# Kernel optimization log

Hardware: AMD Instinct MI355X
Metric: run time of the kernel (lower is better)

Reference implementation:

```python
import jax, jax.numpy as jnp
import numpy as np

EMBED_DIM = 768
NUM_HEADS = 12
PROJ_DIM = EMBED_DIM // NUM_HEADS  # 64
M_FEATURES = 128
EPS = 1e-6


def _orthogonal_projection(key, m, d):
    # Faithful to create_projection_matrix(scaling=0): stacked transposed Q-factors
    # of iid gaussian blocks, rescaled by chi-distributed row norms.
    nb_full_blocks = m // d
    keys = jax.random.split(key, nb_full_blocks + 2)
    blocks = []
    for i in range(nb_full_blocks):
        q, _ = jnp.linalg.qr(jax.random.normal(keys[i], (d, d)))
        blocks.append(q.T)
    rem = m - nb_full_blocks * d
    if rem > 0:
        q, _ = jnp.linalg.qr(jax.random.normal(keys[nb_full_blocks], (d, d)))
        blocks.append(q.T[:rem])
    final = jnp.vstack(blocks)
    multiplier = jnp.linalg.norm(jax.random.normal(keys[-1], (m, d)), axis=1)
    return multiplier[:, None] * final


def setup_inputs() -> dict:
    key = jax.random.key(0)
    ks = jax.random.split(key, 8)
    B, L, E = 4, 4096, EMBED_DIM
    s = 1.0 / np.sqrt(E)
    inp = {
        "x": jax.random.normal(ks[0], (B, L, E), jnp.float32),
        "Wq": jax.random.normal(ks[1], (E, E), jnp.float32) * s,
        "bq": jnp.zeros((E,), jnp.float32),
        "Wk": jax.random.normal(ks[2], (E, E), jnp.float32) * s,
        "bk": jnp.zeros((E,), jnp.float32),
        "Wv": jax.random.normal(ks[3], (E, E), jnp.float32) * s,
        "bv": jnp.zeros((E,), jnp.float32),
        "Wo": jax.random.normal(ks[4], (E, E), jnp.float32) * s,
        "bo": jnp.zeros((E,), jnp.float32),
        "proj": _orthogonal_projection(ks[5], M_FEATURES, PROJ_DIM),
    }
    return inp


def _softmax_kernel(data, projection_matrix):
    # data: [B, L, H, D]; projection_matrix: [M, D]
    data_normalizer = 1.0 / jnp.sqrt(jnp.sqrt(jnp.float32(PROJ_DIM)))
    data = data_normalizer * data
    ratio = 1.0 / jnp.sqrt(jnp.float32(projection_matrix.shape[0]))
    data_dash = jnp.einsum("blhd,md->blhm", data, projection_matrix)
    diag_data = jnp.sum(jnp.square(data), axis=-1, keepdims=True) / 2.0  # [B,L,H,1]
    stab = jnp.max(data_dash, axis=-1, keepdims=True)
    return ratio * (jnp.exp(data_dash - diag_data - stab) + EPS)


def reference(x, Wq, bq, Wk, bk, Wv, bv, Wo, bo, proj):
    B, L, E = x.shape
    H, D = NUM_HEADS, PROJ_DIM

    def split_heads(t):
        return t.reshape(B, L, H, D)

    q = split_heads(x @ Wq + bq)
    k = split_heads(x @ Wk + bk)
    v = split_heads(x @ Wv + bv)

    q_prime = _softmax_kernel(q, proj)  # [B,L,H,M]
    k_prime = _softmax_kernel(k, proj)  # [B,L,H,M]

    # Linear-attention numerator/denominator (O(L) in sequence length).
    kvs = jnp.einsum("blhm,blhd->bhmd", k_prime, v)          # [B,H,M,D]
    num = jnp.einsum("blhm,bhmd->blhd", q_prime, kvs)        # [B,L,H,D]
    ks_sum = jnp.sum(k_prime, axis=1)                         # [B,H,M]
    den = jnp.einsum("blhm,bhm->blh", q_prime, ks_sum)        # [B,L,H]
    attention = num / den[..., None]                          # [B,L,H,D]

    # Faithful to source: transpose to [B,H,L,D] then reshape to [B,-1,E].
    concat = jnp.transpose(attention, (0, 2, 1, 3)).reshape(B, -1, E)
    return concat @ Wo + bo
```

## Files before the change

### kernel.cpp

```cpp
#include <hip/hip_runtime.h>

typedef _Float16 f16;
typedef __attribute__((ext_vector_type(8))) _Float16 half8;
typedef __attribute__((ext_vector_type(4))) _Float16 half4;
typedef __attribute__((ext_vector_type(4))) float f32x4;

#define DEVINL static __device__ __forceinline__

constexpr float NORMALIZER = 0.35355339059327373f;
constexpr float RATIO      = 0.08838834764831845f;
constexpr float FEPS       = 1e-6f;

constexpr size_t OFF_WQKVT = 0;
constexpr size_t OFF_WOT   = OFF_WQKVT + (size_t)2304*768*2;
constexpr size_t OFF_PROJF = OFF_WOT   + (size_t)768*768*2;
constexpr size_t OFF_KS    = OFF_PROJF + (size_t)128*64*2;
constexpr size_t OFF_KSP   = OFF_KS    + (size_t)48*128*4;
constexpr size_t OFF_DEN   = OFF_KSP   + (size_t)48*64*128*4;
constexpr size_t OFF_KVST  = OFF_DEN   + (size_t)48*4096*4;
constexpr size_t OFF_KVSP  = OFF_KVST  + (size_t)48*64*128*2;
constexpr size_t OFF_X16   = OFF_KVSP  + (size_t)8*48*128*64*4;
constexpr size_t OFF_ATT   = OFF_X16;
constexpr size_t OFF_Q16   = OFF_X16 + (size_t)16384*768*2;
constexpr size_t OFF_K16   = OFF_Q16 + (size_t)16384*768*2;
constexpr size_t OFF_VT    = OFF_K16 + (size_t)16384*768*2;
constexpr size_t OFF_KPT   = OFF_VT  + (size_t)16384*768*2;

DEVINL void gload_lds16(const f16* g, f16* lds) {
  __builtin_amdgcn_global_load_lds(
      (const __attribute__((address_space(1))) void*)g,
      (__attribute__((address_space(3))) void*)lds, 16, 0, 0);
}

#define VMCNT(n)  asm volatile("s_waitcnt vmcnt(" #n ")" ::: "memory")
#define LGKMCNT0  asm volatile("s_waitcnt lgkmcnt(0)" ::: "memory")
#define SCHEDB    __builtin_amdgcn_sched_barrier(0)
#define BAR       __builtin_amdgcn_s_barrier()

DEVINL void gemm192_core(const f16* __restrict__ Ag, const f16* __restrict__ Bg,
                         f16* smem, f32x4 (&acc)[8][3], int w, int lane)
{
  constexpr int NT = 12;
  const int wm = w >> 2, wn = w & 3;
  const int c = lane & 15, g16 = lane >> 4;
  const int tid = threadIdx.x;

#pragma unroll
  for (int i = 0; i < 8; ++i)
#pragma unroll
    for (int j = 0; j < 3; ++j)
      acc[i][j] = f32x4{0.f, 0.f, 0.f, 0.f};

  auto SA = [&](int tt, int kh, f16* buf) {
    f16* dst = buf + kh * 8192;
#pragma unroll
    for (int u = 0; u < 2; ++u) {
      const int id = u * 512 + tid;
      const int r = id >> 2, sg = id & 3;
      const int seg = sg ^ ((r >> 1) & 3);
      gload_lds16(Ag + (size_t)r * 768 + tt * 64 + kh * 32 + seg * 8,
                  dst + (u * 512 + w * 64) * 8);
    }
  };
  auto SB = [&](int tt, f16* buf) {
    f16* dst = buf + 16384;
#pragma unroll
    for (int u = 0; u < 3; ++u) {
      const int id = u * 512 + tid;
      const int r = id >> 3, sg = id & 7;
      const int seg = sg ^ (r & 7);
      gload_lds16(Bg + (size_t)r * 768 + tt * 64 + seg * 8,
                  dst + (u * 512 + w * 64) * 8);
    }
  };
  auto RDA = [&](const f16* buf, int kh, int mh, half8 (&av)[4]) {
    const f16* base = buf + kh * 8192;
#pragma unroll
    for (int i = 0; i < 4; ++i) {
      const int r = wm * 128 + mh * 64 + i * 16 + c;
      av[i] = *(const half8*)(base + r * 32 + ((g16 ^ ((r >> 1) & 3)) << 3));
    }
  };
  auto RDB = [&](const f16* buf, int kh, half8 (&bv)[3]) {
#pragma unroll
    for (int j = 0; j < 3; ++j) {
      const int r = wn * 48 + j * 16 + c;
      const int s = kh * 4 + g16;
      bv[j] = *(const half8*)(buf + 16384 + r * 64 + ((s ^ (r & 7)) << 3));
    }
  };

  SA(0, 0, smem); SB(0, smem); SA(0, 1, smem);
  VMCNT(0);
  BAR; SCHEDB;

#pragma unroll 1
  for (int t = 0; t < NT; ++t) {
    f16* bufR = smem + (t & 1) * 28672;
    f16* bufW = smem + ((t & 1) ^ 1) * 28672;
    const bool st = (t + 1) < NT;
    half8 av[4], bv[3];

    RDA(bufR, 0, 0, av); RDB(bufR, 0, bv);
    if (st) SA(t + 1, 0, bufW);
    SCHEDB; BAR; LGKMCNT0; SCHEDB;
    __builtin_amdgcn_s_setprio(1);
#pragma unroll
    for (int i = 0; i < 4; ++i)
#pragma unroll
      for (int j = 0; j < 3; ++j)
        acc[i][j] = __builtin_amdgcn_mfma_f32_16x16x32_f16(av[i], bv[j], acc[i][j], 0, 0, 0);
    __builtin_amdgcn_s_setprio(0);
    BAR; SCHEDB;
    RDA(bufR, 0, 1, av);
    if (st) SB(t + 1, bufW);
    SCHEDB; BAR; LGKMCNT0; SCHEDB;
    __builtin_amdgcn_s_setprio(1);
#pragma unroll
    for (int i = 0; i < 4; ++i)
#pragma unroll
      for (int j = 0; j < 3; ++j)
        acc[4 + i][j] = __builtin_amdgcn_mfma_f32_16x16x32_f16(av[i], bv[j], acc[4 + i][j], 0, 0, 0);
    __builtin_amdgcn_s_setprio(0);
    if (st) { VMCNT(5); } else { VMCNT(0); }
    BAR; SCHEDB;
    RDA(bufR, 1, 0, av); RDB(bufR, 1, bv);
    if (st) SA(t + 1, 1, bufW);
    SCHEDB; BAR; LGKMCNT0; SCHEDB;
    __builtin_amdgcn_s_setprio(1);
#pragma unroll
    for (int i = 0; i < 4; ++i)
#pragma unroll
      for (int j = 0; j < 3; ++j)
        acc[i][j] = __builtin_amdgcn_mfma_f32_16x16x32_f16(av[i], bv[j], acc[i][j], 0, 0, 0);
    __builtin_amdgcn_s_setprio(0);
    BAR; SCHEDB;
    RDA(bufR, 1, 1, av);
    SCHEDB; BAR; LGKMCNT0; SCHEDB;
    __builtin_amdgcn_s_setprio(1);
#pragma unroll
    for (int i = 0; i < 4; ++i)
#pragma unroll
      for (int j = 0; j < 3; ++j)
        acc[4 + i][j] = __builtin_amdgcn_mfma_f32_16x16x32_f16(av[i], bv[j], acc[4 + i][j], 0, 0, 0);
    __builtin_amdgcn_s_setprio(0);
    if (st) { VMCNT(2); }
    BAR; SCHEDB;
  }
}

__global__ __launch_bounds__(512, 2) void k_gemm_qkv5(const f16* __restrict__ X16, const f16* __restrict__ WT,
    const float* __restrict__ bq, const float* __restrict__ bk, const float* __restrict__ bv,
    f16* __restrict__ Qo, f16* __restrict__ Ko, f16* __restrict__ VT)
{
  __shared__ f16 smem[57344];
  f32x4 acc[8][3];
  const int lin = blockIdx.x;
  const int xcd = lin & 7, chunk = lin >> 3;
  const int bx = xcd * 8 + chunk / 12;
  const int by = chunk % 12;
  const int brow0 = bx * 256;
  const int t = threadIdx.x, w = t >> 6, lane = t & 63;
  gemm192_core(X16 + (size_t)brow0 * 768, WT + (size_t)by * 192 * 768, smem, acc, w, lane);

  const int wm = w >> 2, wn = w & 3;
  const int c = lane & 15, g16 = lane >> 4;
  const int which = by >> 2;
  const int colhdr = (by & 3) * 192;
  const float* bias = which == 0 ? bq : (which == 1 ? bk : bv);
  float bb[3];
#pragma unroll
  for (int j = 0; j < 3; ++j) bb[j] = bias[colhdr + wn * 48 + j * 16 + c];

  f16* ep = smem;
  if (which < 2) {
    f16* QK = which == 0 ? Qo : Ko;
#pragma unroll 1
    for (int p = 0; p < 2; ++p) {
      __syncthreads();
      if (wm == p) {
#pragma unroll
        for (int ii = 0; ii < 8; ++ii)
#pragma unroll
          for (int j = 0; j < 3; ++j)
#pragma unroll
            for (int r = 0; r < 4; ++r)
              ep[((ii >> 2) * 64 + (ii & 3) * 16 + g16 * 4 + r) * 200 + wn * 48 + j * 16 + c]
                  = (f16)(acc[ii][j][r] + bb[j]);
      }
      __syncthreads();
      const int row = t >> 2, sg = (t & 3) * 48;
      f16* dst = QK + (size_t)(brow0 + p * 128 + row) * 768 + colhdr + sg;
      const f16* sp = ep + row * 200 + sg;
#pragma unroll
      for (int u = 0; u < 6; ++u) *(half8*)(dst + u * 8) = *(const half8*)(sp + u * 8);
    }
  } else {
    const int bIdx = brow0 >> 12;
#pragma unroll 1
    for (int p = 0; p < 2; ++p) {
      __syncthreads();
      if (wm == p) {
#pragma unroll
        for (int ii = 0; ii < 8; ++ii)
#pragma unroll
          for (int j = 0; j < 3; ++j)
#pragma unroll
            for (int r = 0; r < 4; ++r)
              ep[(wn * 48 + j * 16 + c) * 136 + (ii >> 2) * 64 + (ii & 3) * 16 + g16 * 4 + r]
                  = (f16)(acc[ii][j][r] + bb[j]);
      }
      __syncthreads();
      if (t < 384) {
        const int cl = t >> 1, sg = (t & 1) * 64;
        const int vcol = colhdr + cl;
        const int h = vcol >> 6, d = vcol & 63;
        f16* dst = VT + ((size_t)(bIdx * 12 + h) * 64 + d) * 4096 + (brow0 & 4095) + p * 128 + sg;
        const f16* sp = ep + cl * 136 + sg;
#pragma unroll
        for (int u = 0; u < 8; ++u) *(half8*)(dst + u * 8) = *(const half8*)(sp + u * 8);
      }
    }
  }
}

__global__ __launch_bounds__(512, 2) void k_gemm_out5(const f16* __restrict__ ATT, const f16* __restrict__ WOT,
    const float* __restrict__ bo, float* __restrict__ out)
{
  __shared__ f16 smem[57344];
  f32x4 acc[8][3];
  const int lin = blockIdx.x;
  const int xcd = lin & 7, chunk = lin >> 3;
  const int bx = xcd * 8 + (chunk >> 2);
  const int by = chunk & 3;
  const int brow0 = bx * 256;
  const int t = threadIdx.x, w = t >> 6, lane = t & 63;
  gemm192_core(ATT + (size_t)brow0 * 768, WOT + (size_t)by * 192 * 768, smem, acc, w, lane);

  const int wm = w >> 2, wn = w & 3;
  const int c = lane & 15, g16 = lane >> 4;
  float bb[3];
#pragma unroll
  for (int j = 0; j < 3; ++j) bb[j] = bo[by * 192 + wn * 48 + j * 16 + c];
#pragma unroll
  for (int ii = 0; ii < 8; ++ii) {
    const int row0 = brow0 + wm * 128 + (ii >> 2) * 64 + (ii & 3) * 16 + g16 * 4;
#pragma unroll
    for (int j = 0; j < 3; ++j) {
      const int col = by * 192 + wn * 48 + j * 16 + c;
#pragma unroll
      for (int r = 0; r < 4; ++r)
        out[(size_t)(row0 + r) * 768 + col] = acc[ii][j][r] + bb[j];
    }
  }
}

template<int BN>
DEVINL void gemm_tile(const f16* A, int lda, const f16* Bt, int ldb, int K,
                      f16* As, f16* Bs, f32x4 (&acc)[4][BN/32])
{
  constexpr int NF = BN/32;
  const int t = threadIdx.x;
  const int w = t >> 6, lane = t & 63;
  const int g = lane >> 4, c = lane & 15;
  const int wr = w >> 1, wc = w & 1;
  const int srow = lane >> 2;
  const int sseg = (lane & 3) * 8;

#pragma unroll
  for (int i = 0; i < 4; ++i)
#pragma unroll
    for (int j = 0; j < NF; ++j)
      acc[i][j] = f32x4{0.f, 0.f, 0.f, 0.f};

  for (int k0 = 0; k0 < K; k0 += 32) {
#pragma unroll
    for (int r = 0; r < 2; ++r) {
      const int rowblk = (w + 4*r) * 16;
      gload_lds16(A + (size_t)(rowblk + srow) * lda + k0 + sseg, As + rowblk*32);
    }
#pragma unroll
    for (int r = 0; r < BN/64; ++r) {
      const int rowblk = (w + 4*r) * 16;
      gload_lds16(Bt + (size_t)(rowblk + srow) * ldb + k0 + sseg, Bs + rowblk*32);
    }
    __syncthreads();
    half8 av[4], bv[NF];
#pragma unroll
    for (int i = 0; i < 4; ++i)
      av[i] = *(const half8*)(As + (wr*64 + i*16 + c)*32 + g*8);
#pragma unroll
    for (int j = 0; j < NF; ++j)
      bv[j] = *(const half8*)(Bs + (wc*(BN/2) + j*16 + c)*32 + g*8);
#pragma unroll
    for (int i = 0; i < 4; ++i)
#pragma unroll
      for (int j = 0; j < NF; ++j)
        acc[i][j] = __builtin_amdgcn_mfma_f32_16x16x32_f16(av[i], bv[j], acc[i][j], 0, 0, 0);
    __syncthreads();
  }
}

__global__ __launch_bounds__(256) void k_cast_x(const float* __restrict__ X, f16* __restrict__ X16)
{
  const size_t i = ((size_t)blockIdx.x*256 + threadIdx.x) * 4;
  const float4 v = *(const float4*)(X + i);
  half4 h;
  h[0] = (f16)v.x; h[1] = (f16)v.y; h[2] = (f16)v.z; h[3] = (f16)v.w;
  *(half4*)(X16 + i) = h;
}

__global__ __launch_bounds__(256) void k_transpose_w(const float* __restrict__ W, f16* __restrict__ Wt)
{
  __shared__ float ls[64][65];
  const int t = threadIdx.x;
  const int k0 = blockIdx.x*64, n0 = blockIdx.y*64;
#pragma unroll
  for (int it = 0; it < 4; ++it) {
    const int r = it*16 + (t >> 4);
    const int cs = (t & 15) * 4;
    const float4 v = *(const float4*)(W + (size_t)(k0 + r)*768 + n0 + cs);
    ls[r][cs+0] = v.x; ls[r][cs+1] = v.y; ls[r][cs+2] = v.z; ls[r][cs+3] = v.w;
  }
  __syncthreads();
  const int n = t >> 2;
  const int seg = (t & 3) * 16;
  half8 ov[2];
#pragma unroll
  for (int i = 0; i < 16; ++i) ov[i>>3][i&7] = (f16)ls[seg + i][n];
  f16* dst = Wt + (size_t)(n0 + n)*768 + k0 + seg;
  *(half8*)dst = ov[0];
  *(half8*)(dst + 8) = ov[1];
}

__global__ __launch_bounds__(256) void k_cast_proj(const float* __restrict__ P, f16* __restrict__ PF)
{
  const int i = blockIdx.x*256 + threadIdx.x;
  PF[i] = (f16)(NORMALIZER * P[i]);
}

DEVINL void feat_common(const f16* base, const f16* PROJF,
                        f16* qs, f16* ps, float* dd, float* diag_s)
{
  const int t = threadIdx.x, w = t >> 6, lane = t & 63;
#pragma unroll
  for (int it = 0; it < 2; ++it) {
    const int rowblk = it*32 + w*8;
    gload_lds16(base + (size_t)(rowblk + (lane>>3))*768 + (lane&7)*8, qs + rowblk*64);
  }
#pragma unroll
  for (int it = 0; it < 4; ++it) {
    const int rowblk = it*32 + w*8;
    gload_lds16(PROJF + (size_t)(rowblk + (lane>>3))*64 + (lane&7)*8, ps + rowblk*64);
  }
  __syncthreads();
  if (t < 64) {
    float s = 0.f;
    for (int d = 0; d < 64; ++d) { const float qv = (float)qs[t*64 + d]; s += qv*qv; }
    diag_s[t] = 0.0625f * s;
  }
  const int g = lane >> 4, c = lane & 15;
  const int wr = w >> 1, wc = w & 1;
  f32x4 facc[2][4];
#pragma unroll
  for (int i = 0; i < 2; ++i)
#pragma unroll
    for (int j = 0; j < 4; ++j) facc[i][j] = f32x4{0.f,0.f,0.f,0.f};
#pragma unroll
  for (int kk = 0; kk < 2; ++kk) {
    half8 av[2], bv[4];
#pragma unroll
    for (int i = 0; i < 2; ++i) av[i] = *(const half8*)(qs + (wr*32 + i*16 + c)*64 + kk*32 + g*8);
#pragma unroll
    for (int j = 0; j < 4; ++j) bv[j] = *(const half8*)(ps + (wc*64 + j*16 + c)*64 + kk*32 + g*8);
#pragma unroll
    for (int i = 0; i < 2; ++i)
#pragma unroll
      for (int j = 0; j < 4; ++j)
        facc[i][j] = __builtin_amdgcn_mfma_f32_16x16x32_f16(av[i], bv[j], facc[i][j], 0, 0, 0);
  }
#pragma unroll
  for (int i = 0; i < 2; ++i)
#pragma unroll
    for (int j = 0; j < 4; ++j)
#pragma unroll
      for (int r = 0; r < 4; ++r)
        dd[(wr*32 + i*16 + g*4 + r)*129 + wc*64 + j*16 + c] = facc[i][j][r];
  __syncthreads();
}

__global__ __launch_bounds__(256) void k_kfeat(const f16* __restrict__ Kin, const f16* __restrict__ PROJF,
    f16* __restrict__ KPT, float* __restrict__ KSP)
{
  __shared__ f16 qs[64*64];
  __shared__ f16 ps[128*64];
  __shared__ float dd[64*129];
  __shared__ float diag_s[64];
  const int t = threadIdx.x;
  const int lb = blockIdx.x, bh = blockIdx.y;
  const int b = bh / 12, h = bh - b*12;
  feat_common(Kin + ((size_t)(b*4096 + lb*64))*768 + h*64, PROJF, qs, ps, dd, diag_s);
  const int l = t >> 2, s = t & 3;
  float v[32];
#pragma unroll
  for (int j = 0; j < 32; ++j) v[j] = dd[l*129 + s*32 + j];
  float mx = v[0];
#pragma unroll
  for (int j = 1; j < 32; ++j) mx = fmaxf(mx, v[j]);
  mx = fmaxf(mx, __shfl_xor(mx, 1));
  mx = fmaxf(mx, __shfl_xor(mx, 2));
  const float off = diag_s[l] + mx;
#pragma unroll
  for (int j = 0; j < 32; ++j) dd[l*129 + s*32 + j] = RATIO * (__expf(v[j] - off) + FEPS);
  __syncthreads();
  if (t < 128) {
    float sm = 0.f;
    for (int l2 = 0; l2 < 64; ++l2) sm += dd[l2*129 + t];
    KSP[((size_t)bh*64 + lb)*128 + t] = sm;
  }
  const int m = t >> 1, hf = t & 1;
  half8 ov[4];
#pragma unroll
  for (int i2 = 0; i2 < 32; ++i2) ov[i2>>3][i2&7] = (f16)dd[(hf*32 + i2)*129 + m];
  f16* dst = KPT + ((size_t)bh*128 + m)*4096 + lb*64 + hf*32;
#pragma unroll
  for (int q8 = 0; q8 < 4; ++q8) *(half8*)(dst + q8*8) = ov[q8];
}

__global__ __launch_bounds__(256) void k_kvs(const f16* __restrict__ KPT, const f16* __restrict__ VT,
    float* __restrict__ KVSP)
{
  __shared__ f16 As[128*32], Bs[64*32];
  f32x4 acc[4][2];
  const int chunk = blockIdx.x, bh = blockIdx.y;
  gemm_tile<64>(KPT + (size_t)bh*128*4096 + chunk*512, 4096,
                VT  + (size_t)bh*64*4096  + chunk*512, 4096, 512, As, Bs, acc);
  const int t = threadIdx.x, w = t>>6, lane = t&63, g = lane>>4, c = lane&15;
  const int wr = w>>1, wc = w&1;
  float* dst = KVSP + (size_t)(chunk*48 + bh)*128*64;
#pragma unroll
  for (int i = 0; i < 4; ++i) {
    const int row0 = wr*64 + i*16 + g*4;
#pragma unroll
    for (int j = 0; j < 2; ++j) {
      const int col = wc*32 + j*16 + c;
#pragma unroll
      for (int r = 0; r < 4; ++r) dst[(size_t)(row0 + r)*64 + col] = acc[i][j][r];
    }
  }
}

__global__ __launch_bounds__(256) void k_reduce(const float* __restrict__ KVSP, const float* __restrict__ KSP,
    f16* __restrict__ KVST, float* __restrict__ KS)
{
  const int i = blockIdx.x*256 + threadIdx.x;
  if (i < 48*128*64) {
    const int bh = i >> 13, md = i & 8191, m = md >> 6, d = md & 63;
    float s = 0.f;
#pragma unroll
    for (int c = 0; c < 8; ++c) s += KVSP[((size_t)(c*48 + bh)*128 + m)*64 + d];
    KVST[((size_t)bh*64 + d)*128 + m] = (f16)s;
  }
  if (i < 48*128) {
    const int bh = i >> 7, m = i & 127;
    float s = 0.f;
#pragma unroll 8
    for (int lb = 0; lb < 64; ++lb) s += KSP[((size_t)bh*64 + lb)*128 + m];
    KS[i] = s;
  }
}

__global__ __launch_bounds__(256) void k_qfn(const f16* __restrict__ Q, const f16* __restrict__ PROJF,
    const float* __restrict__ KS, const f16* __restrict__ KVST, f16* __restrict__ ATT)
{
  __shared__ f16 qs[64*64];
  __shared__ f16 ps[128*64];
  __shared__ float dd[64*129];
  __shared__ float diag_s[64];
  __shared__ float den_s[64];
  __shared__ f16 qp[64*128];
  __shared__ float ks_s[128];
  const int t = threadIdx.x;
  const int lb = blockIdx.x, bh = blockIdx.y;
  const int b = bh / 12, h = bh - b*12;
  if (t < 128) ks_s[t] = KS[bh*128 + t];
  feat_common(Q + ((size_t)(b*4096 + lb*64))*768 + h*64, PROJF, qs, ps, dd, diag_s);

  const int w = t >> 6, lane = t & 63, g16 = lane >> 4, c = lane & 15;
  const int wr = w >> 1, wc = w & 1;
  half8 bv2[2][4];
#pragma unroll
  for (int j = 0; j < 2; ++j) {
    const int d = wc*32 + j*16 + c;
#pragma unroll
    for (int kk = 0; kk < 4; ++kk)
      bv2[j][kk] = *(const half8*)(KVST + (size_t)bh*8192 + d*128 + kk*32 + g16*8);
  }

  const int l = t >> 2, s = t & 3;
  float v[32];
#pragma unroll
  for (int j = 0; j < 32; ++j) v[j] = dd[l*129 + s*32 + j];
  float mx = v[0];
#pragma unroll
  for (int j = 1; j < 32; ++j) mx = fmaxf(mx, v[j]);
  mx = fmaxf(mx, __shfl_xor(mx, 1));
  mx = fmaxf(mx, __shfl_xor(mx, 2));
  const float off = diag_s[l] + mx;
  half8 ov[4];
  float dp = 0.f;
#pragma unroll
  for (int j = 0; j < 32; ++j) {
    const float e = RATIO * (__expf(v[j] - off) + FEPS);
    ov[j>>3][j&7] = (f16)e;
    dp += e * ks_s[s*32 + j];
  }
  dp += __shfl_xor(dp, 1);
  dp += __shfl_xor(dp, 2);
  if (s == 0) den_s[l] = dp;
#pragma unroll
  for (int k = 0; k < 4; ++k)
    *(half8*)(qp + l*128 + (((4*s + k) ^ (l & 7)) << 3)) = ov[k];
  __syncthreads();

  f32x4 acc2[2][2];
#pragma unroll
  for (int i = 0; i < 2; ++i)
#pragma unroll
    for (int j = 0; j < 2; ++j) acc2[i][j] = f32x4{0.f,0.f,0.f,0.f};
#pragma unroll
  for (int kk = 0; kk < 4; ++kk) {
    half8 av2[2];
#pragma unroll
    for (int i = 0; i < 2; ++i) {
      const int l2 = wr*32 + i*16 + c;
      av2[i] = *(const half8*)(qp + l2*128 + (((kk*4 + g16) ^ (l2 & 7)) << 3));
    }
#pragma unroll
    for (int i = 0; i < 2; ++i)
#pragma unroll
      for (int j = 0; j < 2; ++j)
        acc2[i][j] = __builtin_amdgcn_mfma_f32_16x16x32_f16(av2[i], bv2[j][kk], acc2[i][j], 0, 0, 0);
  }

  f16* ep = ps;
#pragma unroll
  for (int i = 0; i < 2; ++i)
#pragma unroll
    for (int j = 0; j < 2; ++j)
#pragma unroll
      for (int r = 0; r < 4; ++r) {
        const int l3 = wr*32 + i*16 + g16*4 + r;
        ep[l3*72 + wc*32 + j*16 + c] = (f16)(acc2[i][j][r] / den_s[l3]);
      }
  __syncthreads();
  const int row = t >> 2, sg = (t & 3) * 16;
  f16* dst = ATT + ((size_t)bh*4096 + lb*64 + row)*64 + sg;
  const f16* sp = ep + row*72 + sg;
  *(half8*)dst = *(const half8*)sp;
  *(half8*)(dst + 8) = *(const half8*)(sp + 8);
}

extern "C" void kernel_launch(void* const* d_in, const int* in_sizes, int n_in,
                              void* d_out, int out_size, void* d_ws, size_t ws_size,
                              hipStream_t stream)
{
  const float* x    = (const float*)d_in[0];
  const float* Wq   = (const float*)d_in[1];
  const float* bq   = (const float*)d_in[2];
  const float* Wk   = (const float*)d_in[3];
  const float* bk   = (const float*)d_in[4];
  const float* Wv   = (const float*)d_in[5];
  const float* bv   = (const float*)d_in[6];
  const float* Wo   = (const float*)d_in[7];
  const float* bo   = (const float*)d_in[8];
  const float* proj = (const float*)d_in[9];
  float* out = (float*)d_out;
  char* ws = (char*)d_ws;

  f16*   WQKVT = (f16*)(ws + OFF_WQKVT);
  f16*   WOT   = (f16*)(ws + OFF_WOT);
  f16*   PROJF = (f16*)(ws + OFF_PROJF);
  float* KS    = (float*)(ws + OFF_KS);
  float* KSP   = (float*)(ws + OFF_KSP);
  f16*   KVST  = (f16*)(ws + OFF_KVST);
  float* KVSP  = (float*)(ws + OFF_KVSP);
  f16*   X16   = (f16*)(ws + OFF_X16);
  f16*   ATT   = (f16*)(ws + OFF_ATT);
  f16*   Q16   = (f16*)(ws + OFF_Q16);
  f16*   K16   = (f16*)(ws + OFF_K16);
  f16*   VT    = (f16*)(ws + OFF_VT);
  f16*   KPT   = (f16*)(ws + OFF_KPT);

  k_cast_x<<<12288, 256, 0, stream>>>(x, X16);
  k_transpose_w<<<dim3(12,12), 256, 0, stream>>>(Wq, WQKVT);
  k_transpose_w<<<dim3(12,12), 256, 0, stream>>>(Wk, WQKVT + (size_t)768*768);
  k_transpose_w<<<dim3(12,12), 256, 0, stream>>>(Wv, WQKVT + (size_t)2*768*768);
  k_transpose_w<<<dim3(12,12), 256, 0, stream>>>(Wo, WOT);
  k_cast_proj<<<32, 256, 0, stream>>>(proj, PROJF);

  k_gemm_qkv5<<<768, 512, 0, stream>>>(X16, WQKVT, bq, bk, bv, Q16, K16, VT);
  k_kfeat<<<dim3(64,48), 256, 0, stream>>>(K16, PROJF, KPT, KSP);
  k_kvs<<<dim3(8,48), 256, 0, stream>>>(KPT, VT, KVSP);
  k_reduce<<<1536, 256, 0, stream>>>(KVSP, KSP, KVST, KS);
  k_qfn<<<dim3(64,48), 256, 0, stream>>>(Q16, PROJF, KS, KVST, ATT);
  k_gemm_out5<<<256, 512, 0, stream>>>(ATT, WOT, bo, out);
}
```

Measured before the change: 251.5 us.

## Shrink GEMM tiles to 128 rows, raise occupancy, split KVS chunks, fuse weight transposes

The QKV and output GEMMs move from 256x192 tiles with 64-wide K steps to 128x192 tiles with 32-wide K steps. This cuts LDS and accumulator use so four blocks fit per CU, and launches twice as many blocks for better load balance on the GPU. The pipeline is simplified to one barrier and one vmcnt(0) per K step, dropping the finer-grained scheduling barriers. KVS is also split into 16 sequence chunks instead of 8, and the four weight transposes are merged into one launch. In exchange, the smaller tiles reuse less data per block and the simpler pipeline overlaps loads with compute less.

```diff
diff --git a/kernel.cpp b/kernel.cpp
--- a/kernel.cpp
+++ b/kernel.cpp
@@ -16,10 +16,9 @@
 constexpr size_t OFF_PROJF = OFF_WOT   + (size_t)768*768*2;
 constexpr size_t OFF_KS    = OFF_PROJF + (size_t)128*64*2;
 constexpr size_t OFF_KSP   = OFF_KS    + (size_t)48*128*4;
-constexpr size_t OFF_DEN   = OFF_KSP   + (size_t)48*64*128*4;
-constexpr size_t OFF_KVST  = OFF_DEN   + (size_t)48*4096*4;
+constexpr size_t OFF_KVST  = OFF_KSP   + (size_t)48*64*128*4;
 constexpr size_t OFF_KVSP  = OFF_KVST  + (size_t)48*64*128*2;
-constexpr size_t OFF_X16   = OFF_KVSP  + (size_t)8*48*128*64*4;
+constexpr size_t OFF_X16   = OFF_KVSP  + (size_t)16*48*128*64*4;
 constexpr size_t OFF_ATT   = OFF_X16;
 constexpr size_t OFF_Q16   = OFF_X16 + (size_t)16384*768*2;
 constexpr size_t OFF_K16   = OFF_Q16 + (size_t)16384*768*2;
@@ -32,136 +31,102 @@
       (__attribute__((address_space(3))) void*)lds, 16, 0, 0);
 }
 
-#define VMCNT(n)  asm volatile("s_waitcnt vmcnt(" #n ")" ::: "memory")
-#define LGKMCNT0  asm volatile("s_waitcnt lgkmcnt(0)" ::: "memory")
-#define SCHEDB    __builtin_amdgcn_sched_barrier(0)
+#define VMCNT0    asm volatile("s_waitcnt vmcnt(0)" ::: "memory")
 #define BAR       __builtin_amdgcn_s_barrier()
 
-DEVINL void gemm192_core(const f16* __restrict__ Ag, const f16* __restrict__ Bg,
-                         f16* smem, f32x4 (&acc)[8][3], int w, int lane)
-{
-  constexpr int NT = 12;
+DEVINL void gemm128_core(const f16* __restrict__ Ag, const f16* __restrict__ Bg,
+                         f16* smem, f32x4 (&acc)[4][3], int w, int lane)
+{
+  constexpr int NT = 24;
   const int wm = w >> 2, wn = w & 3;
   const int c = lane & 15, g16 = lane >> 4;
   const int tid = threadIdx.x;
 
 #pragma unroll
-  for (int i = 0; i < 8; ++i)
+  for (int i = 0; i < 4; ++i)
 #pragma unroll
     for (int j = 0; j < 3; ++j)
       acc[i][j] = f32x4{0.f, 0.f, 0.f, 0.f};
 
-  auto SA = [&](int tt, int kh, f16* buf) {
-    f16* dst = buf + kh * 8192;
-#pragma unroll
-    for (int u = 0; u < 2; ++u) {
-      const int id = u * 512 + tid;
+  auto SA = [&](int tt, f16* buf) {
+    const int r = tid >> 2, sg = tid & 3;
+    const int seg = sg ^ ((r >> 1) & 3);
+    gload_lds16(Ag + (size_t)r * 768 + tt * 32 + seg * 8, buf + w * 64 * 8);
+  };
+  auto SB = [&](int tt, f16* buf) {
+    {
+      const int r = tid >> 2, sg = tid & 3;
+      const int seg = sg ^ ((r >> 1) & 3);
+      gload_lds16(Bg + (size_t)r * 768 + tt * 32 + seg * 8, buf + 4096 + w * 64 * 8);
+    }
+    if (w < 4) {
+      const int id = 512 + tid;
       const int r = id >> 2, sg = id & 3;
       const int seg = sg ^ ((r >> 1) & 3);
-      gload_lds16(Ag + (size_t)r * 768 + tt * 64 + kh * 32 + seg * 8,
-                  dst + (u * 512 + w * 64) * 8);
+      gload_lds16(Bg + (size_t)r * 768 + tt * 32 + seg * 8, buf + 4096 + (512 + w * 64) * 8);
     }
   };
-  auto SB = [&](int tt, f16* buf) {
-    f16* dst = buf + 16384;
-#pragma unroll
-    for (int u = 0; u < 3; ++u) {
-      const int id = u * 512 + tid;
-      const int r = id >> 3, sg = id & 7;
-      const int seg = sg ^ (r & 7);
-      gload_lds16(Bg + (size_t)r * 768 + tt * 64 + seg * 8,
-                  dst + (u * 512 + w * 64) * 8);
+  auto RDA = [&](const f16* buf, int mh, half8 (&av)[4]) {
+#pragma unroll
+    for (int i = 0; i < 4; ++i) {
+      const int r = wm * 64 + mh * 32 + i * 16 + c;
+      av[i] = *(const half8*)(buf + r * 32 + ((g16 ^ ((r >> 1) & 3)) << 3));
     }
   };
-  auto RDA = [&](const f16* buf, int kh, int mh, half8 (&av)[4]) {
-    const f16* base = buf + kh * 8192;
-#pragma unroll
-    for (int i = 0; i < 4; ++i) {
-      const int r = wm * 128 + mh * 64 + i * 16 + c;
-      av[i] = *(const half8*)(base + r * 32 + ((g16 ^ ((r >> 1) & 3)) << 3));
-    }
-  };
-  auto RDB = [&](const f16* buf, int kh, half8 (&bv)[3]) {
+  auto RDB = [&](const f16* buf, half8 (&bv)[3]) {
 #pragma unroll
     for (int j = 0; j < 3; ++j) {
       const int r = wn * 48 + j * 16 + c;
-      const int s = kh * 4 + g16;
-      bv[j] = *(const half8*)(buf + 16384 + r * 64 + ((s ^ (r & 7)) << 3));
+      bv[j] = *(const half8*)(buf + 4096 + r * 32 + ((g16 ^ ((r >> 1) & 3)) << 3));
     }
   };
 
-  SA(0, 0, smem); SB(0, smem); SA(0, 1, smem);
-  VMCNT(0);
-  BAR; SCHEDB;
+  SA(0, smem); SB(0, smem);
+  VMCNT0;
+  BAR;
 
 #pragma unroll 1
   for (int t = 0; t < NT; ++t) {
-    f16* bufR = smem + (t & 1) * 28672;
-    f16* bufW = smem + ((t & 1) ^ 1) * 28672;
+    f16* bufR = smem + (t & 1) * 10240;
+    f16* bufW = smem + ((t & 1) ^ 1) * 10240;
     const bool st = (t + 1) < NT;
     half8 av[4], bv[3];
 
-    RDA(bufR, 0, 0, av); RDB(bufR, 0, bv);
-    if (st) SA(t + 1, 0, bufW);
-    SCHEDB; BAR; LGKMCNT0; SCHEDB;
+    RDA(bufR, 0, av); RDB(bufR, bv);
+    if (st) SA(t + 1, bufW);
     __builtin_amdgcn_s_setprio(1);
 #pragma unroll
-    for (int i = 0; i < 4; ++i)
+    for (int i = 0; i < 2; ++i)
 #pragma unroll
       for (int j = 0; j < 3; ++j)
         acc[i][j] = __builtin_amdgcn_mfma_f32_16x16x32_f16(av[i], bv[j], acc[i][j], 0, 0, 0);
     __builtin_amdgcn_s_setprio(0);
-    BAR; SCHEDB;
-    RDA(bufR, 0, 1, av);
     if (st) SB(t + 1, bufW);
-    SCHEDB; BAR; LGKMCNT0; SCHEDB;
     __builtin_amdgcn_s_setprio(1);
 #pragma unroll
-    for (int i = 0; i < 4; ++i)
-#pragma unroll
-      for (int j = 0; j < 3; ++j)
-        acc[4 + i][j] = __builtin_amdgcn_mfma_f32_16x16x32_f16(av[i], bv[j], acc[4 + i][j], 0, 0, 0);
-    __builtin_amdgcn_s_setprio(0);
-    if (st) { VMCNT(5); } else { VMCNT(0); }
-    BAR; SCHEDB;
-    RDA(bufR, 1, 0, av); RDB(bufR, 1, bv);
-    if (st) SA(t + 1, 1, bufW);
-    SCHEDB; BAR; LGKMCNT0; SCHEDB;
-    __builtin_amdgcn_s_setprio(1);
-#pragma unroll
-    for (int i = 0; i < 4; ++i)
+    for (int i = 2; i < 4; ++i)
 #pragma unroll
       for (int j = 0; j < 3; ++j)
         acc[i][j] = __builtin_amdgcn_mfma_f32_16x16x32_f16(av[i], bv[j], acc[i][j], 0, 0, 0);
     __builtin_amdgcn_s_setprio(0);
-    BAR; SCHEDB;
-    RDA(bufR, 1, 1, av);
-    SCHEDB; BAR; LGKMCNT0; SCHEDB;
-    __builtin_amdgcn_s_setprio(1);
-#pragma unroll
-    for (int i = 0; i < 4; ++i)
-#pragma unroll
-      for (int j = 0; j < 3; ++j)
-        acc[4 + i][j] = __builtin_amdgcn_mfma_f32_16x16x32_f16(av[i], bv[j], acc[4 + i][j], 0, 0, 0);
-    __builtin_amdgcn_s_setprio(0);
-    if (st) { VMCNT(2); }
-    BAR; SCHEDB;
-  }
-}
-
-__global__ __launch_bounds__(512, 2) void k_gemm_qkv5(const f16* __restrict__ X16, const f16* __restrict__ WT,
+    VMCNT0;
+    BAR;
+  }
+}
+
+__global__ __launch_bounds__(512, 4) void k_gemm_qkv6(const f16* __restrict__ X16, const f16* __restrict__ WT,
     const float* __restrict__ bq, const float* __restrict__ bk, const float* __restrict__ bv,
     f16* __restrict__ Qo, f16* __restrict__ Ko, f16* __restrict__ VT)
 {
-  __shared__ f16 smem[57344];
-  f32x4 acc[8][3];
+  __shared__ f16 smem[20480];
+  f32x4 acc[4][3];
   const int lin = blockIdx.x;
   const int xcd = lin & 7, chunk = lin >> 3;
-  const int bx = xcd * 8 + chunk / 12;
+  const int bx = xcd * 16 + chunk / 12;
   const int by = chunk % 12;
-  const int brow0 = bx * 256;
-  const int t = threadIdx.x, w = t >> 6, lane = t & 63;
-  gemm192_core(X16 + (size_t)brow0 * 768, WT + (size_t)by * 192 * 768, smem, acc, w, lane);
+  const int brow0 = bx * 128;
+  const int tid = threadIdx.x, w = tid >> 6, lane = tid & 63;
+  gemm128_core(X16 + (size_t)brow0 * 768, WT + (size_t)by * 192 * 768, smem, acc, w, lane);
 
   const int wm = w >> 2, wn = w & 3;
   const int c = lane & 15, g16 = lane >> 4;
@@ -180,62 +145,61 @@
       __syncthreads();
       if (wm == p) {
 #pragma unroll
-        for (int ii = 0; ii < 8; ++ii)
+        for (int i = 0; i < 4; ++i)
 #pragma unroll
           for (int j = 0; j < 3; ++j)
 #pragma unroll
             for (int r = 0; r < 4; ++r)
-              ep[((ii >> 2) * 64 + (ii & 3) * 16 + g16 * 4 + r) * 200 + wn * 48 + j * 16 + c]
-                  = (f16)(acc[ii][j][r] + bb[j]);
+              ep[(i * 16 + g16 * 4 + r) * 200 + wn * 48 + j * 16 + c] = (f16)(acc[i][j][r] + bb[j]);
       }
       __syncthreads();
-      const int row = t >> 2, sg = (t & 3) * 48;
-      f16* dst = QK + (size_t)(brow0 + p * 128 + row) * 768 + colhdr + sg;
-      const f16* sp = ep + row * 200 + sg;
-#pragma unroll
-      for (int u = 0; u < 6; ++u) *(half8*)(dst + u * 8) = *(const half8*)(sp + u * 8);
+      const int row = tid >> 3, c8 = (tid & 7) * 24;
+      f16* dst = QK + (size_t)(brow0 + p * 64 + row) * 768 + colhdr + c8;
+      const f16* sp = ep + row * 200 + c8;
+#pragma unroll
+      for (int u = 0; u < 3; ++u) *(half8*)(dst + u * 8) = *(const half8*)(sp + u * 8);
     }
   } else {
     const int bIdx = brow0 >> 12;
 #pragma unroll 1
-    for (int p = 0; p < 2; ++p) {
+    for (int ch = 0; ch < 2; ++ch) {
       __syncthreads();
-      if (wm == p) {
-#pragma unroll
-        for (int ii = 0; ii < 8; ++ii)
+      if ((wn >> 1) == ch) {
+#pragma unroll
+        for (int i = 0; i < 4; ++i)
 #pragma unroll
           for (int j = 0; j < 3; ++j)
 #pragma unroll
             for (int r = 0; r < 4; ++r)
-              ep[(wn * 48 + j * 16 + c) * 136 + (ii >> 2) * 64 + (ii & 3) * 16 + g16 * 4 + r]
-                  = (f16)(acc[ii][j][r] + bb[j]);
+              ep[((wn & 1) * 48 + j * 16 + c) * 136 + wm * 64 + i * 16 + g16 * 4 + r]
+                  = (f16)(acc[i][j][r] + bb[j]);
       }
       __syncthreads();
-      if (t < 384) {
-        const int cl = t >> 1, sg = (t & 1) * 64;
-        const int vcol = colhdr + cl;
+      if (tid < 384) {
+        const int cl = tid >> 2, sg = (tid & 3) * 32;
+        const int vcol = colhdr + ch * 96 + cl;
         const int h = vcol >> 6, d = vcol & 63;
-        f16* dst = VT + ((size_t)(bIdx * 12 + h) * 64 + d) * 4096 + (brow0 & 4095) + p * 128 + sg;
+        f16* dst = VT + ((size_t)(bIdx * 12 + h) * 64 + d) * 4096 + (brow0 & 4095) + sg;
         const f16* sp = ep + cl * 136 + sg;
 #pragma unroll
-        for (int u = 0; u < 8; ++u) *(half8*)(dst + u * 8) = *(const half8*)(sp + u * 8);
+        for (int u = 0; u < 4; ++u) *(half8*)(dst + u * 8) = *(const half8*)(sp + u * 8);
       }
     }
   }
 }
 
-__global__ __launch_bounds__(512, 2) void k_gemm_out5(const f16* __restrict__ ATT, const f16* __restrict__ WOT,
+__global__ __launch_bounds__(512, 4) void k_gemm_out6(const f16* __restrict__ ATT, const f16* __restrict__ WOT,
     const float* __restrict__ bo, float* __restrict__ out)
 {
-  __shared__ f16 smem[57344];
-  f32x4 acc[8][3];
+  __shared__ f16 smem[20480];
+  f32x4 acc[4][3];
   const int lin = blockIdx.x;
   const int xcd = lin & 7, chunk = lin >> 3;
-  const int bx = xcd * 8 + (chunk >> 2);
+  const int bx = xcd * 16 + (chunk >> 2);
   const int by = chunk & 3;
-  const int brow0 = bx * 256;
-  const int t = threadIdx.x, w = t >> 6, lane = t & 63;
-  gemm192_core(ATT + (size_t)brow0 * 768, WOT + (size_t)by * 192 * 768, smem, acc, w, lane);
+  const int brow0 = bx * 128;
+  const int tid = threadIdx.x, w = tid >> 6, lane = tid & 63;
+  gemm128_core(ATT + (size_t)brow0 * 768, WOT + (size_t)by * 192 * 768, smem, acc, w, lane);
 
   const int wm = w >> 2, wn = w & 3;
   const int c = lane & 15, g16 = lane >> 4;
@@ -243,14 +207,14 @@
 #pragma unroll
   for (int j = 0; j < 3; ++j) bb[j] = bo[by * 192 + wn * 48 + j * 16 + c];
 #pragma unroll
-  for (int ii = 0; ii < 8; ++ii) {
-    const int row0 = brow0 + wm * 128 + (ii >> 2) * 64 + (ii & 3) * 16 + g16 * 4;
+  for (int i = 0; i < 4; ++i) {
+    const int row0 = brow0 + wm * 64 + i * 16 + g16 * 4;
 #pragma unroll
     for (int j = 0; j < 3; ++j) {
       const int col = by * 192 + wn * 48 + j * 16 + c;
 #pragma unroll
       for (int r = 0; r < 4; ++r)
-        out[(size_t)(row0 + r) * 768 + col] = acc[ii][j][r] + bb[j];
+        out[(size_t)(row0 + r) * 768 + col] = acc[i][j][r] + bb[j];
     }
   }
 }
@@ -310,11 +274,14 @@
   *(half4*)(X16 + i) = h;
 }
 
-__global__ __launch_bounds__(256) void k_transpose_w(const float* __restrict__ W, f16* __restrict__ Wt)
+__global__ __launch_bounds__(256) void k_transpose_w4(const float* __restrict__ Wq, const float* __restrict__ Wk,
+    const float* __restrict__ Wv, const float* __restrict__ Wo, f16* __restrict__ WQKVT, f16* __restrict__ WOT)
 {
   __shared__ float ls[64][65];
   const int t = threadIdx.x;
-  const int k0 = blockIdx.x*64, n0 = blockIdx.y*64;
+  const int k0 = blockIdx.x*64, n0 = blockIdx.y*64, z = blockIdx.z;
+  const float* W = z == 0 ? Wq : (z == 1 ? Wk : (z == 2 ? Wv : Wo));
+  f16* Wt = z < 3 ? (WQKVT + (size_t)z*768*768) : WOT;
 #pragma unroll
   for (int it = 0; it < 4; ++it) {
     const int r = it*16 + (t >> 4);
@@ -433,8 +400,8 @@
   __shared__ f16 As[128*32], Bs[64*32];
   f32x4 acc[4][2];
   const int chunk = blockIdx.x, bh = blockIdx.y;
-  gemm_tile<64>(KPT + (size_t)bh*128*4096 + chunk*512, 4096,
-                VT  + (size_t)bh*64*4096  + chunk*512, 4096, 512, As, Bs, acc);
+  gemm_tile<64>(KPT + (size_t)bh*128*4096 + chunk*256, 4096,
+                VT  + (size_t)bh*64*4096  + chunk*256, 4096, 256, As, Bs, acc);
   const int t = threadIdx.x, w = t>>6, lane = t&63, g = lane>>4, c = lane&15;
   const int wr = w>>1, wc = w&1;
   float* dst = KVSP + (size_t)(chunk*48 + bh)*128*64;
@@ -458,7 +425,7 @@
     const int bh = i >> 13, md = i & 8191, m = md >> 6, d = md & 63;
     float s = 0.f;
 #pragma unroll
-    for (int c = 0; c < 8; ++c) s += KVSP[((size_t)(c*48 + bh)*128 + m)*64 + d];
+    for (int c = 0; c < 16; ++c) s += KVSP[((size_t)(c*48 + bh)*128 + m)*64 + d];
     KVST[((size_t)bh*64 + d)*128 + m] = (f16)s;
   }
   if (i < 48*128) {
@@ -593,16 +560,13 @@
   f16*   KPT   = (f16*)(ws + OFF_KPT);
 
   k_cast_x<<<12288, 256, 0, stream>>>(x, X16);
-  k_transpose_w<<<dim3(12,12), 256, 0, stream>>>(Wq, WQKVT);
-  k_transpose_w<<<dim3(12,12), 256, 0, stream>>>(Wk, WQKVT + (size_t)768*768);
-  k_transpose_w<<<dim3(12,12), 256, 0, stream>>>(Wv, WQKVT + (size_t)2*768*768);
-  k_transpose_w<<<dim3(12,12), 256, 0, stream>>>(Wo, WOT);
+  k_transpose_w4<<<dim3(12,12,4), 256, 0, stream>>>(Wq, Wk, Wv, Wo, WQKVT, WOT);
   k_cast_proj<<<32, 256, 0, stream>>>(proj, PROJF);
 
-  k_gemm_qkv5<<<768, 512, 0, stream>>>(X16, WQKVT, bq, bk, bv, Q16, K16, VT);
+  k_gemm_qkv6<<<1536, 512, 0, stream>>>(X16, WQKVT, bq, bk, bv, Q16, K16, VT);
   k_kfeat<<<dim3(64,48), 256, 0, stream>>>(K16, PROJF, KPT, KSP);
-  k_kvs<<<dim3(8,48), 256, 0, stream>>>(KPT, VT, KVSP);
+  k_kvs<<<dim3(16,48), 256, 0, stream>>>(KPT, VT, KVSP);
   k_reduce<<<1536, 256, 0, stream>>>(KVSP, KSP, KVST, KS);
   k_qfn<<<dim3(64,48), 256, 0, stream>>>(Q16, PROJF, KS, KVST, ATT);
-  k_gemm_out5<<<256, 512, 0, stream>>>(ATT, WOT, bo, out);
-}
+  k_gemm_out6<<<512, 512, 0, stream>>>(ATT, WOT, bo, out);
+}
```

Measured after the change: 255.5 us. About the same (+1.6%).
